# Kernel tuning notes

Measured on AMD Instinct MI355X. Metric: run time of the kernel, lower is better.

Reference implementation:

```python
import jax, jax.numpy as jnp
import numpy as np

B, N, M, D = 32, 1024, 1024, 128  # pairs, nodes in X-graph, nodes in Y-graph, feature dim


def setup_inputs() -> dict:
    key = jax.random.key(0)
    k0, k1, k2, k3 = jax.random.split(key, 4)
    return {
        "Xs": jax.random.normal(k0, (B, N, D), dtype=jnp.float32),
        "Ys": jax.random.normal(k1, (B, M, D), dtype=jnp.float32),
        "weights": jax.random.normal(k2, (B, N, D), dtype=jnp.float32),
        "A_w": jax.random.normal(k3, (D, D), dtype=jnp.float32) / np.sqrt(D).astype(np.float32),
        "A_b": jnp.zeros((D,), dtype=jnp.float32),
    }


def reference(Xs, Ys, weights, A_w, A_b):
    # coefficients = tanh(Linear(W))  -> [B, N, D]
    coeff = jnp.tanh(jnp.einsum("bnd,ed->bne", weights, A_w) + A_b)
    # affinity: softplus((X * coeff) @ Y^T) - 0.5  -> [B, N, M]
    s = jax.nn.softplus(jnp.einsum("bnd,bmd->bnm", Xs * coeff, Ys)) - 0.5
    # dual-direction attention
    a_x = jax.nn.softmax(s, axis=2)   # row softmax (dim=1 on [N,M])
    a_y = jax.nn.softmax(s, axis=1)   # col softmax (dim=0 on [N,M])
    attention_x = jnp.einsum("bnm,bmd->bnd", a_x, Ys)   # a_x @ Y
    attention_y = jnp.einsum("bnm,bnd->bmd", a_y, Xs)   # a_y^T @ X
    return attention_x, attention_y, s
```

## Files before the change

kernel.cpp:

```cpp
#include <hip/hip_runtime.h>
#include <hip/hip_bf16.h>

#define BB 32
#define NN 1024
#define MM 1024
#define DD 128

typedef __bf16 bf16;
typedef bf16 bf16x8 __attribute__((ext_vector_type(8)));
typedef bf16 bf16x4 __attribute__((ext_vector_type(4)));
typedef float f32x4 __attribute__((ext_vector_type(4)));

#define LOG2E 1.4426950408889634f
#define LN2   0.6931471805599453f
#define ESHIFT 30.5f
#define ESHIFT_C 5.6757e-14f

__device__ __forceinline__ bf16x8 ld8(const bf16* p) {
    return *reinterpret_cast<const bf16x8*>(p);
}

__device__ __forceinline__ bf16x8 cvt8(const float* p) {
    float4 a = reinterpret_cast<const float4*>(p)[0];
    float4 c = reinterpret_cast<const float4*>(p)[1];
    bf16x8 r;
    r[0]=(bf16)a.x; r[1]=(bf16)a.y; r[2]=(bf16)a.z; r[3]=(bf16)a.w;
    r[4]=(bf16)c.x; r[5]=(bf16)c.y; r[6]=(bf16)c.z; r[7]=(bf16)c.w;
    return r;
}

__global__ void k_prep(const float* __restrict__ Xs, const float* __restrict__ Ys,
                       bf16* __restrict__ Ysb, bf16* __restrict__ YsT,
                       bf16* __restrict__ XsT) {
    __shared__ float tile[32][129];
    int b = blockIdx.y;
    int yy = blockIdx.x;
    int isY = (yy < 32);
    int r0 = (yy & 31) * 32;
    const float* s = (isY ? Ys : Xs) + (size_t)b * 1024 * DD;
    int tid = threadIdx.x;
    int c4 = (tid & 31) * 4;
#pragma unroll
    for (int p = 0; p < 4; ++p) {
        int r = p * 8 + (tid >> 5);
        float4 v = *reinterpret_cast<const float4*>(s + (size_t)(r0 + r) * DD + c4);
        tile[r][c4] = v.x; tile[r][c4 + 1] = v.y; tile[r][c4 + 2] = v.z; tile[r][c4 + 3] = v.w;
        if (isY) {
            bf16x4 o; o[0] = (bf16)v.x; o[1] = (bf16)v.y; o[2] = (bf16)v.z; o[3] = (bf16)v.w;
            *reinterpret_cast<bf16x4*>(Ysb + (size_t)b * MM * DD + (size_t)(r0 + r) * DD + c4) = o;
        }
    }
    __syncthreads();
    bf16* dT = (isY ? YsT : XsT) + (size_t)b * DD * 1024;
    int c = tid >> 1, rh = (tid & 1) * 16;
    bf16x8 o0, o1;
#pragma unroll
    for (int j = 0; j < 8; ++j) o0[j] = (bf16)tile[rh + j][c];
#pragma unroll
    for (int j = 0; j < 8; ++j) o1[j] = (bf16)tile[rh + 8 + j][c];
    *reinterpret_cast<bf16x8*>(dT + (size_t)c * 1024 + r0 + rh) = o0;
    *reinterpret_cast<bf16x8*>(dT + (size_t)c * 1024 + r0 + rh + 8) = o1;
}

__global__ __launch_bounds__(256) void k_coeff(
    const float* __restrict__ Xs, const float* __restrict__ W,
    const float* __restrict__ Aw, const float* __restrict__ Ab,
    bf16* __restrict__ Xc) {
    int ntile = blockIdx.x, b = blockIdx.y;
    int tid = threadIdx.x;
    int w = tid >> 6, lane = tid & 63, quad = lane >> 4, l16 = lane & 15;
    int nbase = ntile * 64 + w * 16;

    f32x4 accZ[8];
#pragma unroll
    for (int ef = 0; ef < 8; ++ef) accZ[ef] = {0.f, 0.f, 0.f, 0.f};

    const float* Wb = W + ((size_t)b * NN + nbase + l16) * DD;
#pragma unroll
    for (int ks = 0; ks < 4; ++ks) {
        bf16x8 aW = cvt8(Wb + ks * 32 + quad * 8);
#pragma unroll
        for (int ef = 0; ef < 8; ++ef) {
            bf16x8 bA = cvt8(Aw + (size_t)(ef * 16 + l16) * DD + ks * 32 + quad * 8);
            accZ[ef] = __builtin_amdgcn_mfma_f32_16x16x32_bf16(aW, bA, accZ[ef], 0, 0, 0);
        }
    }
#pragma unroll
    for (int ef = 0; ef < 8; ++ef) {
        float ab = Ab[ef * 16 + l16];
#pragma unroll
        for (int r = 0; r < 4; ++r) {
            float z = accZ[ef][r] + ab;
            z = fminf(fmaxf(z, -12.f), 12.f);
            float t = __builtin_amdgcn_exp2f(z * (2.f * LOG2E));
            float c = (t - 1.f) / (t + 1.f);
            int n = nbase + quad * 4 + r;
            size_t idx = ((size_t)b * NN + n) * DD + ef * 16 + l16;
            Xc[idx] = (bf16)(Xs[idx] * c);
        }
    }
}

__global__ __launch_bounds__(256, 2) void k_main(
    const bf16* __restrict__ Xc, const bf16* __restrict__ Ysb,
    const bf16* __restrict__ YsT, const bf16* __restrict__ XsT,
    float* __restrict__ out_x, float* __restrict__ out_y,
    float* __restrict__ out_s) {
    __shared__ __align__(16) bf16 stage[2][16384];
    __shared__ __align__(16) bf16 Et[4][16][72];

    int L = blockIdx.x + 32 * blockIdx.y;
    int xcd = L & 7, sidx = L >> 3;
    int b = xcd + 8 * (sidx & 3);
    int t = sidx >> 2;
    int role = t >> 4, tile = t & 15;
    int tid = threadIdx.x;
    int w = tid >> 6, lane = tid & 63, quad = lane >> 4, l16 = lane & 15;
    int rbase = tile * 64 + w * 16;

    const bf16* Arow  = (role == 0 ? Xc : Ysb) + ((size_t)b * 1024 + rbase + l16) * DD;
    const bf16* Bmat  = (role == 0 ? Ysb : Xc) + (size_t)b * 1024 * DD;
    const bf16* BTmat = (role == 0 ? YsT : XsT) + (size_t)b * DD * 1024;
    float* s_b = out_s + (size_t)b * NN * MM;
    float* outp = (role == 0 ? out_x : out_y);

    bf16x8 aX[4];
#pragma unroll
    for (int ks = 0; ks < 4; ++ks) aX[ks] = ld8(Arow + ks * 32 + quad * 8);

    int isA = (w < 2);
    uint32_t wroff[8], soff[8];
#pragma unroll
    for (int i = 0; i < 8; ++i) {
        uint32_t o = (uint32_t)(w * 8 + i) * 1024 + (uint32_t)lane * 16;
        if (isA) {
            wroff[i] = o ^ (((o >> 8) & 7) << 4);
            soff[i]  = o;
        } else {
            uint32_t j = o - 16384;
            wroff[i] = 16384 + (j ^ (((j >> 7) & 7) << 4));
            soff[i]  = (j >> 7) * 2048 + (j & 127);
        }
    }
    const char* srcbase = (const char*)(isA ? Bmat : BTmat);
    uint32_t tstride = isA ? 16384u : 128u;

    bf16x8 stg[8];
#pragma unroll
    for (int i = 0; i < 8; ++i)
        stg[i] = *reinterpret_cast<const bf16x8*>(srcbase + soff[i]);
#pragma unroll
    for (int i = 0; i < 8; ++i)
        *reinterpret_cast<bf16x8*>((char*)&stage[0][0] + wroff[i]) = stg[i];
    __syncthreads();

    f32x4 accU[8];
#pragma unroll
    for (int df = 0; df < 8; ++df) accU[df] = {0.f, 0.f, 0.f, 0.f};
    float rowsum[4] = {0.f, 0.f, 0.f, 0.f};
    uint32_t xq = (uint32_t)(l16 & 7) << 4;
    int cur = 0;

#pragma unroll 1
    for (int tt = 0; tt < 16; ++tt) {
        if (tt < 15) {
#pragma unroll
            for (int i = 0; i < 8; ++i)
                stg[i] = *reinterpret_cast<const bf16x8*>(srcbase + (size_t)(tt + 1) * tstride + soff[i]);
        }
        __builtin_amdgcn_sched_barrier(0);

        const char* sb = (const char*)&stage[cur][0];
        f32x4 accS[4];
#pragma unroll
        for (int mf = 0; mf < 4; ++mf) accS[mf] = {0.f, 0.f, 0.f, 0.f};
#pragma unroll
        for (int ks = 0; ks < 4; ++ks) {
            bf16x8 bY[4];
#pragma unroll
            for (int mf = 0; mf < 4; ++mf)
                bY[mf] = *reinterpret_cast<const bf16x8*>(
                    sb + (uint32_t)(mf * 16 + l16) * 256 + (((uint32_t)(ks * 64 + quad * 16)) ^ xq));
#pragma unroll
            for (int mf = 0; mf < 4; ++mf)
                accS[mf] = __builtin_amdgcn_mfma_f32_16x16x32_bf16(aX[ks], bY[mf], accS[mf], 0, 0, 0);
        }
#pragma unroll
        for (int mf = 0; mf < 4; ++mf) {
#pragma unroll
            for (int r = 0; r < 4; ++r) {
                float x = accS[mf][r];
                float E = __builtin_amdgcn_exp2f((x - ESHIFT) * LOG2E) + ESHIFT_C;
                bf16 Eb = (bf16)E;
                rowsum[r] += (float)Eb;
                Et[w][quad * 4 + r][mf * 16 + l16] = Eb;
            }
            if (role == 0) {
#pragma unroll
                for (int r = 0; r < 4; ++r) {
                    float x = accS[mf][r];
                    float ax = fabsf(x);
                    float sp = fmaxf(x, 0.f) +
                               LN2 * __builtin_amdgcn_logf(1.f + __builtin_amdgcn_exp2f(-ax * LOG2E));
                    s_b[(size_t)(rbase + quad * 4 + r) * MM + tt * 64 + mf * 16 + l16] = sp - 0.5f;
                }
            }
        }
#pragma unroll
        for (int half = 0; half < 2; ++half) {
            bf16x8 aE = *reinterpret_cast<const bf16x8*>(&Et[w][l16][half * 32 + quad * 8]);
            bf16x8 bT[8];
#pragma unroll
            for (int df = 0; df < 8; ++df)
                bT[df] = *reinterpret_cast<const bf16x8*>(
                    sb + 16384 + (uint32_t)(df * 16 + l16) * 128 + (((uint32_t)(half * 64 + quad * 16)) ^ xq));
#pragma unroll
            for (int df = 0; df < 8; ++df)
                accU[df] = __builtin_amdgcn_mfma_f32_16x16x32_bf16(aE, bT[df], accU[df], 0, 0, 0);
        }
        __builtin_amdgcn_sched_barrier(0);
        if (tt < 15) {
#pragma unroll
            for (int i = 0; i < 8; ++i)
                *reinterpret_cast<bf16x8*>((char*)&stage[cur ^ 1][0] + wroff[i]) = stg[i];
        }
        __builtin_amdgcn_sched_barrier(0);
        asm volatile("s_waitcnt lgkmcnt(0)" ::: "memory");
        __builtin_amdgcn_s_barrier();
        __builtin_amdgcn_sched_barrier(0);
        cur ^= 1;
    }

    float inv[4];
#pragma unroll
    for (int r = 0; r < 4; ++r) {
        float rs = rowsum[r];
        rs += __shfl_xor(rs, 1); rs += __shfl_xor(rs, 2);
        rs += __shfl_xor(rs, 4); rs += __shfl_xor(rs, 8);
        inv[r] = 1.f / rs;
    }
#pragma unroll
    for (int df = 0; df < 8; ++df)
#pragma unroll
        for (int r = 0; r < 4; ++r)
            outp[((size_t)b * 1024 + rbase + quad * 4 + r) * DD + df * 16 + l16] = accU[df][r] * inv[r];
}

extern "C" void kernel_launch(void* const* d_in, const int* in_sizes, int n_in,
                              void* d_out, int out_size, void* d_ws, size_t ws_size,
                              hipStream_t stream) {
    const float* Xs = (const float*)d_in[0];
    const float* Ys = (const float*)d_in[1];
    const float* W  = (const float*)d_in[2];
    const float* Aw = (const float*)d_in[3];
    const float* Ab = (const float*)d_in[4];

    char* ws = (char*)d_ws;
    bf16*  Xc     = (bf16*)(ws);
    bf16*  Ysb    = (bf16*)(ws + 8388608);
    bf16*  YsT    = (bf16*)(ws + 16777216);
    bf16*  XsT    = (bf16*)(ws + 25165824);

    float* out_x = (float*)d_out;
    float* out_y = out_x + (size_t)BB * NN * DD;
    float* out_s = out_y + (size_t)BB * MM * DD;

    k_prep<<<dim3(64, BB), 256, 0, stream>>>(Xs, Ys, Ysb, YsT, XsT);
    k_coeff<<<dim3(NN / 64, BB), 256, 0, stream>>>(Xs, W, Aw, Ab, Xc);
    k_main<<<dim3(32, BB), 256, 0, stream>>>(Xc, Ysb, YsT, XsT, out_x, out_y, out_s);
}
```

Before: 293.6 us.

## Retile prep transpose, stage coeff through LDS for coalesced stores, XCD-aware block mapping

The prep kernel now transposes 64x64 tiles instead of 32x128 strips, so each thread writes one 16-byte transposed chunk per pass. The coeff kernel stages the tanh coefficients in shared memory, then reads Xs and writes Xc with vectorized, coalesced row accesses instead of scattered 2-byte stores. Both kernels switch to a 1D grid whose block-to-batch mapping follows the XCD interleave used by the main kernel, aiming for better L2 locality. The cost is extra LDS use and a barrier in the coeff kernel.

```diff
diff --git a/kernel.cpp b/kernel.cpp
--- a/kernel.cpp
+++ b/kernel.cpp
@@ -29,44 +29,56 @@
     return r;
 }
 
-__global__ void k_prep(const float* __restrict__ Xs, const float* __restrict__ Ys,
-                       bf16* __restrict__ Ysb, bf16* __restrict__ YsT,
-                       bf16* __restrict__ XsT) {
-    __shared__ float tile[32][129];
-    int b = blockIdx.y;
-    int yy = blockIdx.x;
-    int isY = (yy < 32);
-    int r0 = (yy & 31) * 32;
-    const float* s = (isY ? Ys : Xs) + (size_t)b * 1024 * DD;
+__global__ __launch_bounds__(256) void k_prep(
+    const float* __restrict__ Xs, const float* __restrict__ Ys,
+    bf16* __restrict__ Ysb, bf16* __restrict__ YsT, bf16* __restrict__ XsT) {
+    __shared__ float tile[64][65];
+    int L = blockIdx.x;
+    int xcd = L & 7, sidx = L >> 3;
+    int b = xcd + 8 * (sidx & 3);
+    int t = sidx >> 2;
+    int isY = (t < 32);
+    int tt = t & 31;
+    int mtile = tt >> 1, dtile = tt & 1;
+    int r0 = mtile * 64, d0 = dtile * 64;
     int tid = threadIdx.x;
-    int c4 = (tid & 31) * 4;
+    const float* src = (isY ? Ys : Xs) + (size_t)b * 1024 * DD;
+
+    int rr = tid >> 4;
+    int c4 = (tid & 15) * 4;
 #pragma unroll
     for (int p = 0; p < 4; ++p) {
-        int r = p * 8 + (tid >> 5);
-        float4 v = *reinterpret_cast<const float4*>(s + (size_t)(r0 + r) * DD + c4);
-        tile[r][c4] = v.x; tile[r][c4 + 1] = v.y; tile[r][c4 + 2] = v.z; tile[r][c4 + 3] = v.w;
+        int row = p * 16 + rr;
+        float4 v = *reinterpret_cast<const float4*>(src + (size_t)(r0 + row) * DD + d0 + c4);
+        tile[row][c4] = v.x; tile[row][c4 + 1] = v.y;
+        tile[row][c4 + 2] = v.z; tile[row][c4 + 3] = v.w;
         if (isY) {
             bf16x4 o; o[0] = (bf16)v.x; o[1] = (bf16)v.y; o[2] = (bf16)v.z; o[3] = (bf16)v.w;
-            *reinterpret_cast<bf16x4*>(Ysb + (size_t)b * MM * DD + (size_t)(r0 + r) * DD + c4) = o;
+            *reinterpret_cast<bf16x4*>(Ysb + (size_t)b * MM * DD + (size_t)(r0 + row) * DD + d0 + c4) = o;
         }
     }
     __syncthreads();
     bf16* dT = (isY ? YsT : XsT) + (size_t)b * DD * 1024;
-    int c = tid >> 1, rh = (tid & 1) * 16;
-    bf16x8 o0, o1;
-#pragma unroll
-    for (int j = 0; j < 8; ++j) o0[j] = (bf16)tile[rh + j][c];
-#pragma unroll
-    for (int j = 0; j < 8; ++j) o1[j] = (bf16)tile[rh + 8 + j][c];
-    *reinterpret_cast<bf16x8*>(dT + (size_t)c * 1024 + r0 + rh) = o0;
-    *reinterpret_cast<bf16x8*>(dT + (size_t)c * 1024 + r0 + rh + 8) = o1;
+#pragma unroll
+    for (int q = 0; q < 2; ++q) {
+        int d = q * 32 + (tid >> 3);
+        int m0 = (tid & 7) * 8;
+        bf16x8 o;
+#pragma unroll
+        for (int j = 0; j < 8; ++j) o[j] = (bf16)tile[m0 + j][d];
+        *reinterpret_cast<bf16x8*>(dT + (size_t)(d0 + d) * 1024 + r0 + m0) = o;
+    }
 }
 
 __global__ __launch_bounds__(256) void k_coeff(
     const float* __restrict__ Xs, const float* __restrict__ W,
     const float* __restrict__ Aw, const float* __restrict__ Ab,
     bf16* __restrict__ Xc) {
-    int ntile = blockIdx.x, b = blockIdx.y;
+    __shared__ bf16 cf[64][136];
+    int L = blockIdx.x;
+    int xcd = L & 7, sidx = L >> 3;
+    int b = xcd + 8 * (sidx & 3);
+    int ntile = sidx >> 2;
     int tid = threadIdx.x;
     int w = tid >> 6, lane = tid & 63, quad = lane >> 4, l16 = lane & 15;
     int nbase = ntile * 64 + w * 16;
@@ -94,10 +106,25 @@
             z = fminf(fmaxf(z, -12.f), 12.f);
             float t = __builtin_amdgcn_exp2f(z * (2.f * LOG2E));
             float c = (t - 1.f) / (t + 1.f);
-            int n = nbase + quad * 4 + r;
-            size_t idx = ((size_t)b * NN + n) * DD + ef * 16 + l16;
-            Xc[idx] = (bf16)(Xs[idx] * c);
-        }
+            cf[w * 16 + quad * 4 + r][ef * 16 + l16] = (bf16)c;
+        }
+    }
+    __syncthreads();
+    const float* Xs_b = Xs + ((size_t)b * NN + ntile * 64) * DD;
+    bf16* Xc_b = Xc + ((size_t)b * NN + ntile * 64) * DD;
+    int row = tid >> 4, colg = (tid & 15) * 8;
+#pragma unroll
+    for (int p = 0; p < 4; ++p) {
+        int rrow = p * 16 + row;
+        float4 xa = *reinterpret_cast<const float4*>(Xs_b + (size_t)rrow * DD + colg);
+        float4 xb = *reinterpret_cast<const float4*>(Xs_b + (size_t)rrow * DD + colg + 4);
+        bf16x8 cv = *reinterpret_cast<const bf16x8*>(&cf[rrow][colg]);
+        bf16x8 o;
+        o[0] = (bf16)(xa.x * (float)cv[0]); o[1] = (bf16)(xa.y * (float)cv[1]);
+        o[2] = (bf16)(xa.z * (float)cv[2]); o[3] = (bf16)(xa.w * (float)cv[3]);
+        o[4] = (bf16)(xb.x * (float)cv[4]); o[5] = (bf16)(xb.y * (float)cv[5]);
+        o[6] = (bf16)(xb.z * (float)cv[6]); o[7] = (bf16)(xb.w * (float)cv[7]);
+        *reinterpret_cast<bf16x8*>(Xc_b + (size_t)rrow * DD + colg) = o;
     }
 }
 
@@ -265,7 +292,7 @@
     float* out_y = out_x + (size_t)BB * NN * DD;
     float* out_s = out_y + (size_t)BB * MM * DD;
 
-    k_prep<<<dim3(64, BB), 256, 0, stream>>>(Xs, Ys, Ysb, YsT, XsT);
-    k_coeff<<<dim3(NN / 64, BB), 256, 0, stream>>>(Xs, W, Aw, Ab, Xc);
+    k_prep<<<dim3(2048), 256, 0, stream>>>(Xs, Ys, Ysb, YsT, XsT);
+    k_coeff<<<dim3(512), 256, 0, stream>>>(Xs, W, Aw, Ab, Xc);
     k_main<<<dim3(32, BB), 256, 0, stream>>>(Xc, Ysb, YsT, XsT, out_x, out_y, out_s);
 }
```

Measured after the change: 279.9 us. 4.7% less time.
